# Kernel tuning notes

Hardware: AMD Instinct MI355X
Metric: run time of the kernel (lower is better)

The kernel has to match this reference:

```python
import math
import jax, jax.numpy as jnp
import numpy as np

B, S, CNN_D, LLM_D, BR_D, H = 4, 1024, 512, 768, 1024, 16
PW, CW = 0.2, 0.15  # physics_weight, conservation_weight


def _ln(x, g, b, eps=1e-5):
    m = jnp.mean(x, axis=-1, keepdims=True)
    v = jnp.var(x, axis=-1, keepdims=True)
    return (x - m) * jax.lax.rsqrt(v + eps) * g + b


def _mha(x, wqkv, bqkv, wo, bo, h=H):
    # torch nn.MultiheadAttention (batch_first, self-attention, eval mode)
    Bb, Ss, E = x.shape
    d = E // h
    qkv = x @ wqkv.T + bqkv
    q, k, v = jnp.split(qkv, 3, axis=-1)
    sh = lambda t: t.reshape(Bb, Ss, h, d).transpose(0, 2, 1, 3)
    q, k, v = sh(q), sh(k), sh(v)
    a = jax.nn.softmax(jnp.einsum('bhqd,bhkd->bhqk', q, k) / math.sqrt(d), axis=-1)
    o = jnp.einsum('bhqk,bhkd->bhqd', a, v).transpose(0, 2, 1, 3).reshape(Bb, Ss, E)
    return o @ wo.T + bo


def _phys_attn(qx, kx, wq, bq, wk, bk, wv, bv, wo, bo, g, be, h=H):
    # PhysicsInformedAttention._physics_attention (requires Sq == Sk for the bias broadcast)
    Bb, Sq, E = qx.shape
    Sk = kx.shape[1]
    d = E // h
    Q = (qx @ wq.T + bq).reshape(Bb, Sq, h, d).transpose(0, 2, 1, 3)
    K = (kx @ wk.T + bk).reshape(Bb, Sk, h, d).transpose(0, 2, 1, 3)
    V = (kx @ wv.T + bv).reshape(Bb, Sk, h, d).transpose(0, 2, 1, 3)
    scores = jnp.einsum('bhqd,bhkd->bhqk', Q, K) / math.sqrt(d)
    energy_bias = jnp.sum(Q * K, axis=-1, keepdims=True) * PW   # [B,H,S,1]
    mass_bias = jnp.mean(Q + K, axis=-1, keepdims=True) * CW    # [B,H,S,1]
    a = jax.nn.softmax(scores + energy_bias + mass_bias, axis=-1)
    o = jnp.einsum('bhqk,bhkd->bhqd', a, V).transpose(0, 2, 1, 3).reshape(Bb, Sq, E)
    return _ln(qx + (o @ wo.T + bo), g, be)


def _bridge(x, w, b, g, be):
    # Linear -> GELU (exact) -> LayerNorm (Dropout is no-op in eval)
    return _ln(jax.nn.gelu(x @ w.T + b, approximate=False), g, be)


def setup_inputs() -> dict:
    key = jax.random.key(0)
    ks = iter(jax.random.split(key, 64))
    nrm = lambda *s: jax.random.normal(next(ks), s, jnp.float32)
    w = lambda *s: nrm(*s) * 0.02
    return dict(
        datacube=nrm(B, 5, 8, 16, 16),
        llm_features=nrm(B, S, LLM_D),
        enhanced_cnn_features=nrm(B, S, CNN_D),
        sa_wqkv=w(3 * CNN_D, CNN_D), sa_bqkv=jnp.zeros(3 * CNN_D),
        sa_wo=w(CNN_D, CNN_D), sa_bo=jnp.zeros(CNN_D),
        ta_wqkv=w(3 * CNN_D, CNN_D), ta_bqkv=jnp.zeros(3 * CNN_D),
        ta_wo=w(CNN_D, CNN_D), ta_bo=jnp.zeros(CNN_D),
        c2b_w=w(BR_D, CNN_D), c2b_b=jnp.zeros(BR_D), c2b_g=jnp.ones(BR_D), c2b_be=jnp.zeros(BR_D),
        l2b_w=w(BR_D, LLM_D), l2b_b=jnp.zeros(BR_D), l2b_g=jnp.ones(BR_D), l2b_be=jnp.zeros(BR_D),
        pq_w=w(BR_D, BR_D), pq_b=jnp.zeros(BR_D),
        pk_w=w(BR_D, BR_D), pk_b=jnp.zeros(BR_D),
        pv_w=w(BR_D, BR_D), pv_b=jnp.zeros(BR_D),
        po_w=w(BR_D, BR_D), po_b=jnp.zeros(BR_D),
        e_emb=nrm(1, 1, BR_D), m_emb=nrm(1, 1, BR_D), p_emb=nrm(1, 1, BR_D),
        pa_g=jnp.ones(BR_D), pa_be=jnp.zeros(BR_D),
        c2l_w=w(LLM_D, BR_D), c2l_b=jnp.zeros(LLM_D), c2l_g=jnp.ones(LLM_D), c2l_be=jnp.zeros(LLM_D),
        l2c_w=w(CNN_D, BR_D), l2c_b=jnp.zeros(CNN_D), l2c_g=jnp.ones(CNN_D), l2c_be=jnp.zeros(CNN_D),
    )


def reference(datacube, llm_features, enhanced_cnn_features,
              sa_wqkv, sa_bqkv, sa_wo, sa_bo,
              ta_wqkv, ta_bqkv, ta_wo, ta_bo,
              c2b_w, c2b_b, c2b_g, c2b_be,
              l2b_w, l2b_b, l2b_g, l2b_be,
              pq_w, pq_b, pk_w, pk_b, pv_w, pv_b, po_w, po_b,
              e_emb, m_emb, p_emb, pa_g, pa_be,
              c2l_w, c2l_b, c2l_g, c2l_be,
              l2c_w, l2c_b, l2c_g, l2c_be):
    # enhanced_cnn_features path bypasses the conv3d processor
    cnn = enhanced_cnn_features                       # [B,S,512]
    cnn = cnn + _mha(cnn, sa_wqkv, sa_bqkv, sa_wo, sa_bo)   # spatial integration
    cnn = cnn + _mha(cnn, ta_wqkv, ta_bqkv, ta_wo, ta_bo)   # temporal integration
    cnn_b = _bridge(cnn, c2b_w, c2b_b, c2b_g, c2b_be)       # [B,S,1024]
    llm_b = _bridge(llm_features, l2b_w, l2b_b, l2b_g, l2b_be)  # [B,S,1024]
    phys = jnp.broadcast_to(jnp.concatenate([e_emb, m_emb, p_emb], axis=1),
                            (cnn.shape[0], 3, BR_D))
    aug_cnn = jnp.concatenate([cnn_b, phys], axis=1)  # [B,S+3,1024]
    aug_llm = jnp.concatenate([llm_b, phys], axis=1)
    cnn_att = _phys_attn(aug_cnn, aug_llm, pq_w, pq_b, pk_w, pk_b, pv_w, pv_b,
                         po_w, po_b, pa_g, pa_be)[:, :S]
    llm_att = _phys_attn(aug_llm, aug_cnn, pq_w, pq_b, pk_w, pk_b, pv_w, pv_b,
                         po_w, po_b, pa_g, pa_be)[:, :S]
    llm_enhanced = _bridge(cnn_att, c2l_w, c2l_b, c2l_g, c2l_be)  # cnn->llm bridge [B,S,768]
    cnn_enhanced = _bridge(llm_att, l2c_w, l2c_b, l2c_g, l2c_be)  # llm->cnn bridge [B,S,512]
    return (cnn_enhanced, llm_enhanced)
```

## Files before the change

kernel.cpp:

```cpp
#include <hip/hip_runtime.h>
#include <cstdint>
#include <cstddef>

#define B_    4
#define S_    1024
#define CNN_DIM 512
#define LLM_DIM 768
#define BR_DIM  1024
#define NH    16
#define SAUG  1027

typedef __attribute__((ext_vector_type(8))) short short8;
typedef __attribute__((ext_vector_type(4))) float f32x4;
typedef __attribute__((ext_vector_type(4))) unsigned short us4;
typedef unsigned short u16;
typedef unsigned int u32;
typedef unsigned long long u64;

__device__ __forceinline__ float bf2f(u16 h) {
    union { u32 u; float f; } c; c.u = ((u32)h) << 16; return c.f;
}
__device__ __forceinline__ u16 f2bf(float f) {
    union { u32 u; float f; } c; c.f = f;
    return (u16)((c.u + 0x7FFFu + ((c.u >> 16) & 1u)) >> 16);
}
__device__ __forceinline__ short f2bfS(float f) { return (short)f2bf(f); }
__device__ __forceinline__ u32 cvt_pk_bf16(float lo, float hi) {
    u32 r;
    asm("v_cvt_pk_bf16_f32 %0, %1, %2" : "=v"(r) : "v"(lo), "v"(hi));
    return r;
}

#define GLLDS(gp, lp) __builtin_amdgcn_global_load_lds( \
    (const __attribute__((address_space(1))) void*)(gp), \
    (__attribute__((address_space(3))) void*)(lp), 16, 0, 0)

#define NCONV 14
struct ConvArgs { const float* src[NCONV]; u16* dst[NCONV]; int cum[NCONV + 1]; };

__global__ __launch_bounds__(256) void convert_many(ConvArgs a, int total4) {
    int idx = blockIdx.x * 256 + threadIdx.x;
    if (idx >= total4) return;
    int seg = 0;
#pragma unroll
    for (int i = 1; i < NCONV; i++) if (a.cum[i] <= idx) seg = i;
    int j = idx - a.cum[seg];
    float4 v = ((const float4*)a.src[seg])[j];
    us4 o;
    o[0] = f2bf(v.x); o[1] = f2bf(v.y); o[2] = f2bf(v.z); o[3] = f2bf(v.w);
    ((us4*)a.dst[seg])[j] = o;
}

template<int RESID>
__global__ __launch_bounds__(256) void gemm2_kernel(
    const u16* __restrict__ A, const u16* __restrict__ W,
    const float* __restrict__ bias, const void* __restrict__ residp,
    u16* __restrict__ C, int M, int N, int K)
{
    __shared__ u16 smA[2][64 * 64];
    __shared__ u16 smB[2][128 * 64];

    const int tid = threadIdx.x;
    const int lane = tid & 63;
    const int w = tid >> 6;
    const int wm = w & 1, wn = w >> 1;
    const int mi = lane & 15, g = lane >> 4;
    const int m0 = blockIdx.y * 64;
    const int n0 = blockIdx.x * 128;
    const int lrow = lane >> 3;
    const int lcol = lane & 7;

    f32x4 acc[2][4] = {};
    const int nk = K >> 6;
    int cur = 0;

    auto stage = [&](int buf, int kt) {
        const int kbase = kt * 64;
#pragma unroll
        for (int i = 0; i < 6; i++) {
            int c = w * 6 + i;
            if (c < 8) {
                int row = c * 8 + lrow;
                int col16 = lcol ^ (row & 7);
                int grow = m0 + row; if (grow > M - 1) grow = M - 1;
                GLLDS(A + (size_t)grow * K + kbase + col16 * 8, &smA[buf][c * 512]);
            } else {
                int c8 = c - 8;
                int row = c8 * 8 + lrow;
                int col16 = lcol ^ (row & 7);
                GLLDS(W + (size_t)(n0 + row) * K + kbase + col16 * 8, &smB[buf][c8 * 512]);
            }
        }
    };

    stage(0, 0);
    __syncthreads();

    for (int kt = 0; kt < nk; ++kt) {
        if (kt + 1 < nk) stage(cur ^ 1, kt + 1);
#pragma unroll
        for (int h = 0; h < 2; h++) {
            short8 af[2], bf[4];
#pragma unroll
            for (int im = 0; im < 2; im++) {
                int row = wm * 32 + im * 16 + mi;
                af[im] = *(const short8*)&smA[cur][row * 64 + ((h * 4 + g) ^ (mi & 7)) * 8];
            }
#pragma unroll
            for (int in = 0; in < 4; in++) {
                int row = wn * 64 + in * 16 + mi;
                bf[in] = *(const short8*)&smB[cur][row * 64 + ((h * 4 + g) ^ (mi & 7)) * 8];
            }
#pragma unroll
            for (int im = 0; im < 2; im++)
#pragma unroll
                for (int in = 0; in < 4; in++)
                    acc[im][in] = __builtin_amdgcn_mfma_f32_16x16x32_bf16(af[im], bf[in], acc[im][in], 0, 0, 0);
        }
        __syncthreads();
        cur ^= 1;
    }

#pragma unroll
    for (int im = 0; im < 2; im++) {
#pragma unroll
        for (int r = 0; r < 4; r++) {
            int row = m0 + wm * 32 + im * 16 + g * 4 + r;
            if (row >= M) continue;
            size_t base = (size_t)row * N;
#pragma unroll
            for (int in = 0; in < 4; in++) {
                int col = n0 + wn * 64 + in * 16 + mi;
                float v = acc[im][in][r] + bias[col];
                if (RESID == 1) v += bf2f(((const u16*)residp)[base + col]);
                if (RESID == 2) v += ((const float*)residp)[base + col];
                C[base + col] = f2bf(v);
            }
        }
    }
}

template<int DH, bool SPLIT>
__global__ __launch_bounds__(256) void transpose_v(
    const u16* __restrict__ Vin, u16* __restrict__ VTa, u16* __restrict__ VTb,
    int Sk, int in_rs, long long in_bs, int KPAD)
{
    __shared__ u16 tile[64][DH + 8];
    const int tid = threadIdx.x;
    const int gb = blockIdx.z, h = blockIdx.y;
    const int k0 = blockIdx.x * 64;
    const u16* src = Vin + (size_t)gb * in_bs + h * DH;

    constexpr int CH = DH / 8;
    for (int i = tid; i < 64 * CH; i += 256) {
        int key = i / CH, c = i % CH;
        short8 v = {0,0,0,0,0,0,0,0};
        if (k0 + key < Sk) v = *(const short8*)(src + (size_t)(k0 + key) * in_rs + c * 8);
        *(short8*)&tile[key][c * 8] = v;
    }
    __syncthreads();

    u16* base;
    if (SPLIT) base = (gb < 4) ? (VTa + ((size_t)(gb * NH + h) * DH) * KPAD)
                               : (VTb + ((size_t)((gb - 4) * NH + h) * DH) * KPAD);
    else       base = VTa + ((size_t)(gb * NH + h) * DH) * KPAD;
    u16* dst = base + k0;
    for (int i = tid; i < DH * 8; i += 256) {
        int d = i >> 3, c = i & 7;
        short8 o;
#pragma unroll
        for (int j = 0; j < 8; j++) o[j] = (short)tile[c * 8 + j][d];
        *(short8*)(dst + (size_t)d * KPAD + c * 8) = o;
    }
}

template<int DH, bool PHYS>
__global__ __launch_bounds__(256) void attn7(
    const u16* __restrict__ Q, const u16* __restrict__ Kb,
    const u16* __restrict__ VTa, const u16* __restrict__ VTb,
    u16* __restrict__ Ob, int Sk, int q_rs, int kv_rs, int o_rs,
    long long q_bs, long long kv_bs, long long o_bs, int KPAD, float scale)
{
    constexpr int KT = 32;
    constexpr int NDB = DH / 16;
    constexpr int NCH = DH / 32;
    constexpr int KLDP = DH + 8;
    constexpr int VLDP = 40;
    __shared__ __align__(16) u16 Kt[KT][KLDP];
    __shared__ __align__(16) u16 Vt[DH][VLDP];
    __shared__ __align__(16) u64 Px[4][16][10];

    const int tid = threadIdx.x;
    const int lane = tid & 63;
    const int w = tid >> 6;
    const int mi = lane & 15, g = lane >> 4;
    const int z = blockIdx.z, h = blockIdx.y;
    const int hoff = h * DH;
    const int qw = blockIdx.x * 64 + w * 16;
    const float sc2 = scale * 1.44269504088896f;

    int kb, vg;
    const u16* vts;
    if (PHYS) {
        kb = (z < 4) ? z + 4 : z - 4;
        vts = (z < 4) ? VTb : VTa;
        vg = (z < 4) ? z : z - 4;
    } else { kb = z; vts = VTa; vg = z; }

    int krow, kseg; bool kact;
    int vd, vks;   bool vact;
    if (DH == 64) { krow = tid >> 3; kseg = tid & 7; kact = true;
                    vd = tid >> 2;   vks = tid & 3;  vact = true; }
    else          { krow = tid >> 2; kseg = tid & 3; kact = (tid < 128);
                    vd = (tid - 128) >> 2; vks = tid & 3; vact = (tid >= 128); }

    short8 qfrag[NCH];
    {
        const u16* qs = Q + (size_t)z * q_bs + (size_t)(qw + mi) * q_rs + hoff + g * 8;
#pragma unroll
        for (int c = 0; c < NCH; c++) {
            short8 q8 = *(const short8*)(qs + 32 * c);
#pragma unroll
            for (int j = 0; j < 8; j++) q8[j] = f2bfS(bf2f((u16)q8[j]) * sc2);
            qfrag[c] = q8;
        }
    }

    const short one = (short)0x3F80;
    const short8 ones8 = {one, one, one, one, one, one, one, one};

    f32x4 acc[NDB] = {};
    f32x4 accl = {0.f, 0.f, 0.f, 0.f};
    const u16* kbb = Kb + (size_t)kb * kv_bs + hoff;
    const u16* vtb = vts + ((size_t)(vg * NH + h) * DH) * KPAD;

    const int nt = (Sk + KT - 1) / KT;

    short8 kr8 = {0,0,0,0,0,0,0,0}, vr8 = {0,0,0,0,0,0,0,0};
    auto loadKV = [&](int t) {
        if (kact) {
            int key = t * KT + krow; if (key > Sk - 1) key = Sk - 1;
            kr8 = *(const short8*)(kbb + (size_t)key * kv_rs + kseg * 8);
        }
        if (vact)
            vr8 = *(const short8*)(vtb + (size_t)vd * KPAD + t * KT + vks * 8);
    };

    loadKV(0);

    for (int t = 0; t < nt; t++) {
        const int rem = Sk - t * KT;
        __syncthreads();
        if (kact) *(short8*)&Kt[krow][kseg * 8] = kr8;
        if (vact) *(short8*)&Vt[vd][vks * 8] = vr8;
        __syncthreads();
        if (t + 1 < nt) loadKV(t + 1);

        f32x4 sA = {0,0,0,0}, sB = {0,0,0,0};
#pragma unroll
        for (int c = 0; c < NCH; c++) {
            short8 ka = *(const short8*)&Kt[mi][g * 8 + 32 * c];
            short8 kb8 = *(const short8*)&Kt[16 + mi][g * 8 + 32 * c];
            sA = __builtin_amdgcn_mfma_f32_16x16x32_bf16(ka, qfrag[c], sA, 0, 0, 0);
            sB = __builtin_amdgcn_mfma_f32_16x16x32_bf16(kb8, qfrag[c], sB, 0, 0, 0);
        }

        float pa[4], pb[4];
        if (rem >= KT) {
#pragma unroll
            for (int r = 0; r < 4; r++) {
                pa[r] = exp2f(sA[r]);
                pb[r] = exp2f(sB[r]);
            }
        } else {
#pragma unroll
            for (int r = 0; r < 4; r++) {
                pa[r] = (4 * g + r < rem)      ? exp2f(sA[r]) : 0.f;
                pb[r] = (16 + 4 * g + r < rem) ? exp2f(sB[r]) : 0.f;
            }
        }

        {
            uint2 wa, wb;
            wa.x = cvt_pk_bf16(pa[0], pa[1]);
            wa.y = cvt_pk_bf16(pa[2], pa[3]);
            wb.x = cvt_pk_bf16(pb[0], pb[1]);
            wb.y = cvt_pk_bf16(pb[2], pb[3]);
            uint2* prow = (uint2*)&Px[w][mi][0];
            prow[g] = wa;
            prow[4 + g] = wb;
        }
        short8 pfrag = *(const short8*)((const u16*)&Px[w][mi][0] + 8 * g);

        accl = __builtin_amdgcn_mfma_f32_16x16x32_bf16(ones8, pfrag, accl, 0, 0, 0);

#pragma unroll
        for (int db = 0; db < NDB; db++) {
            short8 vf = *(const short8*)&Vt[db * 16 + mi][g * 8];
            acc[db] = __builtin_amdgcn_mfma_f32_16x16x32_bf16(vf, pfrag, acc[db], 0, 0, 0);
        }
    }

    const float inv = 1.f / accl[0];
    u16* obase = Ob + (size_t)z * o_bs + (size_t)(qw + mi) * o_rs + hoff;
#pragma unroll
    for (int db = 0; db < NDB; db++)
#pragma unroll
        for (int r = 0; r < 4; r++)
            obase[db * 16 + 4 * g + r] = f2bf(acc[db][r] * inv);
}

template<bool GELU, bool RESID, bool OUTF32>
__global__ __launch_bounds__(256) void ln_kernel(
    const u16* __restrict__ X, const u16* __restrict__ resid,
    const float* __restrict__ gg, const float* __restrict__ be,
    void* __restrict__ out, int N, int rows_per_batch,
    long long resid_bs, int resid_rs, long long out_bs, int out_rs)
{
    __shared__ float buf[1024];
    __shared__ float red[2][4];
    __shared__ float stat[2];
    const int row = blockIdx.x;
    const int b = row / rows_per_batch, r = row % rows_per_batch;
    const int tid = threadIdx.x, lane = tid & 63, w = tid >> 6;
    const u16* xr = X + (size_t)row * N;
    const u16* rr = RESID ? (resid + (size_t)b * resid_bs + (size_t)r * resid_rs) : (const u16*)nullptr;

    float s = 0.f, s2 = 0.f;
    for (int i0 = tid * 4; i0 < N; i0 += 1024) {
        us4 xv = *(const us4*)(xr + i0);
        us4 rv = {0,0,0,0};
        if (RESID) rv = *(const us4*)(rr + i0);
        float4 xb;
        float* xp = &xb.x;
#pragma unroll
        for (int u = 0; u < 4; u++) {
            float x = bf2f(xv[u]);
            if (RESID) x += bf2f(rv[u]);
            if (GELU)  x = 0.5f * x * (1.f + erff(x * 0.70710678118654752f));
            xp[u] = x; s += x; s2 += x * x;
        }
        *(float4*)&buf[i0] = xb;
    }
#pragma unroll
    for (int off = 32; off; off >>= 1) { s += __shfl_xor(s, off); s2 += __shfl_xor(s2, off); }
    if (lane == 0) { red[0][w] = s; red[1][w] = s2; }
    __syncthreads();
    if (tid == 0) {
        float a = red[0][0] + red[0][1] + red[0][2] + red[0][3];
        float q = red[1][0] + red[1][1] + red[1][2] + red[1][3];
        float mean = a / N;
        float var = q / N - mean * mean;
        stat[0] = mean; stat[1] = rsqrtf(var + 1e-5f);
    }
    __syncthreads();
    const float mean = stat[0], rs = stat[1];
    const size_t obase = (size_t)b * out_bs + (size_t)r * out_rs;
    for (int i0 = tid * 4; i0 < N; i0 += 1024) {
        if (OUTF32) {
            float4 o;
            o.x = (buf[i0+0] - mean) * rs * gg[i0+0] + be[i0+0];
            o.y = (buf[i0+1] - mean) * rs * gg[i0+1] + be[i0+1];
            o.z = (buf[i0+2] - mean) * rs * gg[i0+2] + be[i0+2];
            o.w = (buf[i0+3] - mean) * rs * gg[i0+3] + be[i0+3];
            *(float4*)((float*)out + obase + i0) = o;
        } else {
            us4 o;
#pragma unroll
            for (int u = 0; u < 4; u++)
                o[u] = f2bf((buf[i0+u] - mean) * rs * gg[i0+u] + be[i0+u]);
            *(us4*)((u16*)out + obase + i0) = o;
        }
    }
}

__global__ __launch_bounds__(256) void fill_phys_kernel(
    const float* __restrict__ e, const float* __restrict__ m, const float* __restrict__ p,
    u16* __restrict__ augc, u16* __restrict__ augl)
{
    int i = blockIdx.x * 256 + threadIdx.x;
    if (i >= 3 * BR_DIM) return;
    int r = i / BR_DIM, j = i % BR_DIM;
    u16 v = f2bf((r == 0) ? e[j] : (r == 1) ? m[j] : p[j]);
#pragma unroll
    for (int b = 0; b < B_; b++) {
        size_t off = ((size_t)b * SAUG + S_ + r) * BR_DIM + j;
        augc[off] = v; augl[off] = v;
    }
}

template<int RESID>
static void gemm(hipStream_t s, const u16* A, const u16* W, const float* bias,
                 const void* resid, u16* C, int M, int N, int K)
{
    dim3 grid(N / 128, (M + 63) / 64), block(256);
    gemm2_kernel<RESID><<<grid, block, 0, s>>>(A, W, bias, resid, C, M, N, K);
}

extern "C" void kernel_launch(void* const* d_in, const int* in_sizes, int n_in,
                              void* d_out, int out_size, void* d_ws, size_t ws_size,
                              hipStream_t stream)
{
    auto F = [&](int i) { return (const float*)d_in[i]; };
    uint8_t* ws = (uint8_t*)d_ws;

    u16* W_SA_QKV = (u16*)(ws + 256);
    u16* W_SA_O   = (u16*)(ws + 1573120);
    u16* W_TA_QKV = (u16*)(ws + 2097408);
    u16* W_TA_O   = (u16*)(ws + 3670272);
    u16* W_C2B    = (u16*)(ws + 4194560);
    u16* W_L2B    = (u16*)(ws + 5243136);
    u16* W_PQ     = (u16*)(ws + 6816000);
    u16* W_PK     = (u16*)(ws + 8913152);
    u16* W_PV     = (u16*)(ws + 11010304);
    u16* W_PO     = (u16*)(ws + 13107456);
    u16* W_C2L    = (u16*)(ws + 15204608);
    u16* W_L2C    = (u16*)(ws + 16777472);
    u16* VT32     = (u16*)(ws + 17826048);
    u16* CNN_B    = (u16*)(ws + 17826048);
    u16* LLM_B    = (u16*)(ws + 22020352);
    u16* QKV      = (u16*)(ws + 28311808);
    u16* ATT      = (u16*)(ws + 40894720);
    u16* CNN1     = (u16*)(ws + 45089024);
    u16* CNN2     = (u16*)(ws + 49283328);
    u16* AUGC     = (u16*)(ws + 53477632);
    u16* AUGL     = (u16*)(ws + 61890816);
    u16* VTA      = (u16*)(ws + 17826048);
    u16* PV_ALL   = (u16*)(ws + 26738944);
    u16* VTB      = (u16*)(ws + 43565312);
    u16* OB_ALL   = (u16*)(ws + 26738944);
    u16* PQ_ALL   = (u16*)(ws + 70304000);
    u16* PK_ALL   = (u16*)(ws + 87130368);
    u16* X8       = QKV;
    u16* X8_ALL   = (u16*)(ws + 70304000);
    u16* CATT_ALL = (u16*)(ws + 87130368);
    u16* X6       = (u16*)(ws + 26738944);
    u16* X4       = (u16*)(ws + 26738944);
    float* outp   = (float*)d_out;

    ConvArgs ca;
    const float* srcs[NCONV] = { F(1), F(2), F(3), F(5), F(7), F(9), F(11),
                                 F(15), F(19), F(21), F(23), F(25), F(32), F(36) };
    u16* dsts[NCONV] = { LLM_B, CNN_B, W_SA_QKV, W_SA_O, W_TA_QKV, W_TA_O, W_C2B,
                         W_L2B, W_PQ, W_PK, W_PV, W_PO, W_C2L, W_L2C };
    const int ns[NCONV] = { 3145728, 2097152, 786432, 262144, 786432, 262144, 524288,
                            786432, 1048576, 1048576, 1048576, 1048576, 786432, 524288 };
    int cum = 0;
    for (int i = 0; i < NCONV; i++) { ca.src[i] = srcs[i]; ca.dst[i] = dsts[i]; ca.cum[i] = cum; cum += ns[i] / 4; }
    ca.cum[NCONV] = cum;
    convert_many<<<(cum + 255) / 256, 256, 0, stream>>>(ca, cum);

    const int M4 = B_ * S_;
    const int MA = B_ * SAUG;
    const float sc32 = 0.17677669529663687f;
    const float sc64 = 0.125f;
    const long long bsQKV = (long long)S_ * 3 * CNN_DIM;
    const long long bsATT = (long long)S_ * CNN_DIM;
    const long long bsAUG = (long long)SAUG * BR_DIM;
    const long long bsO   = (long long)S_ * BR_DIM;
    const int KP32 = 1024;
    const int KP64 = 1088;
    dim3 ablock(256);
    dim3 agrid4(S_ / 64, NH, B_), agrid8(S_ / 64, NH, 2 * B_);
    dim3 tgrid32(16, NH, B_), tgrid64(17, NH, 2 * B_);

    gemm<0>(stream, CNN_B, W_SA_QKV, F(4), nullptr, QKV, M4, 3 * CNN_DIM, CNN_DIM);
    transpose_v<32, false><<<tgrid32, 256, 0, stream>>>(QKV + 2 * CNN_DIM, VT32, nullptr, S_, 3 * CNN_DIM, bsQKV, KP32);
    attn7<32, false><<<agrid4, ablock, 0, stream>>>(QKV, QKV + CNN_DIM, VT32, nullptr, ATT,
        S_, 3 * CNN_DIM, 3 * CNN_DIM, CNN_DIM, bsQKV, bsQKV, bsATT, KP32, sc32);
    gemm<2>(stream, ATT, W_SA_O, F(6), F(2), CNN1, M4, CNN_DIM, CNN_DIM);

    gemm<0>(stream, CNN1, W_TA_QKV, F(8), nullptr, QKV, M4, 3 * CNN_DIM, CNN_DIM);
    transpose_v<32, false><<<tgrid32, 256, 0, stream>>>(QKV + 2 * CNN_DIM, VT32, nullptr, S_, 3 * CNN_DIM, bsQKV, KP32);
    attn7<32, false><<<agrid4, ablock, 0, stream>>>(QKV, QKV + CNN_DIM, VT32, nullptr, ATT,
        S_, 3 * CNN_DIM, 3 * CNN_DIM, CNN_DIM, bsQKV, bsQKV, bsATT, KP32, sc32);
    gemm<1>(stream, ATT, W_TA_O, F(10), CNN1, CNN2, M4, CNN_DIM, CNN_DIM);

    gemm<0>(stream, LLM_B, W_L2B, F(16), nullptr, X8, M4, BR_DIM, LLM_DIM);
    ln_kernel<true, false, false><<<M4, 256, 0, stream>>>(X8, nullptr, F(17), F(18), AUGL,
        BR_DIM, S_, 0, 0, bsAUG, BR_DIM);
    gemm<0>(stream, CNN2, W_C2B, F(12), nullptr, X8, M4, BR_DIM, CNN_DIM);
    ln_kernel<true, false, false><<<M4, 256, 0, stream>>>(X8, nullptr, F(13), F(14), AUGC,
        BR_DIM, S_, 0, 0, bsAUG, BR_DIM);
    fill_phys_kernel<<<12, 256, 0, stream>>>(F(27), F(28), F(29), AUGC, AUGL);

    gemm<0>(stream, AUGC, W_PQ, F(20), nullptr, PQ_ALL, 2 * MA, BR_DIM, BR_DIM);
    gemm<0>(stream, AUGC, W_PK, F(22), nullptr, PK_ALL, 2 * MA, BR_DIM, BR_DIM);
    gemm<0>(stream, AUGC, W_PV, F(24), nullptr, PV_ALL, 2 * MA, BR_DIM, BR_DIM);
    transpose_v<64, true><<<tgrid64, 256, 0, stream>>>(PV_ALL, VTA, VTB, SAUG, BR_DIM, bsAUG, KP64);

    attn7<64, true><<<agrid8, ablock, 0, stream>>>(PQ_ALL, PK_ALL, VTA, VTB, OB_ALL,
        SAUG, BR_DIM, BR_DIM, BR_DIM, bsAUG, bsAUG, bsO, KP64, sc64);

    gemm<0>(stream, OB_ALL, W_PO, F(26), nullptr, X8_ALL, 2 * M4, BR_DIM, BR_DIM);
    ln_kernel<false, true, false><<<2 * M4, 256, 0, stream>>>(X8_ALL, AUGC, F(30), F(31), CATT_ALL,
        BR_DIM, S_, bsAUG, BR_DIM, bsO, BR_DIM);

    gemm<0>(stream, CATT_ALL, W_C2L, F(33), nullptr, X6, M4, LLM_DIM, BR_DIM);
    ln_kernel<true, false, true><<<M4, 256, 0, stream>>>(X6, nullptr, F(34), F(35),
        (void*)(outp + 2097152), LLM_DIM, S_, 0, 0, (long long)S_ * LLM_DIM, LLM_DIM);
    gemm<0>(stream, CATT_ALL + (size_t)M4 * BR_DIM, W_L2C, F(37), nullptr, X4, M4, CNN_DIM, BR_DIM);
    ln_kernel<true, false, true><<<M4, 256, 0, stream>>>(X4, nullptr, F(38), F(39),
        (void*)outp, CNN_DIM, S_, 0, 0, (long long)S_ * CNN_DIM, CNN_DIM);
}
```

Measured before the change: 471.4 us.

## Add 128x128 GEMM tile for large M and process two query groups per attention block

Adds a gemm3 kernel with 128x128 tiles, double-buffered LDS loads and XOR-swizzled shared memory, used when M >= 8192 (the physics projection GEMMs with 2*B*(S+3) rows). The attention kernel now handles two 64-query groups per block, reusing each K/V tile loaded into LDS across both groups and halving the attention grid. Both changes aim to cut global/LDS traffic per FLOP. In exchange they raise register pressure and lower block counts, which may reduce occupancy.

```diff
diff --git a/kernel.cpp b/kernel.cpp
--- a/kernel.cpp
+++ b/kernel.cpp
@@ -140,6 +140,95 @@
     }
 }
 
+template<int RESID>
+__global__ __launch_bounds__(256) void gemm3_kernel(
+    const u16* __restrict__ A, const u16* __restrict__ W,
+    const float* __restrict__ bias, const void* __restrict__ residp,
+    u16* __restrict__ C, int M, int N, int K)
+{
+    __shared__ u16 smA[2][128 * 64];
+    __shared__ u16 smB[2][128 * 64];
+
+    const int tid = threadIdx.x;
+    const int lane = tid & 63;
+    const int w = tid >> 6;
+    const int wm = w & 1, wn = w >> 1;
+    const int mi = lane & 15, g = lane >> 4;
+    const int m0 = blockIdx.y * 128;
+    const int n0 = blockIdx.x * 128;
+    const int lrow = lane >> 3;
+    const int lcol = lane & 7;
+
+    f32x4 acc[4][4] = {};
+    const int nk = K >> 6;
+    int cur = 0;
+
+    auto stage = [&](int buf, int kt) {
+        const int kbase = kt * 64;
+#pragma unroll
+        for (int i = 0; i < 4; i++) {
+            int c = w * 4 + i;
+            int row = c * 8 + lrow;
+            int col16 = lcol ^ (row & 7);
+            int grow = m0 + row; if (grow > M - 1) grow = M - 1;
+            GLLDS(A + (size_t)grow * K + kbase + col16 * 8, &smA[buf][c * 512]);
+        }
+#pragma unroll
+        for (int i = 0; i < 4; i++) {
+            int c = w * 4 + i;
+            int row = c * 8 + lrow;
+            int col16 = lcol ^ (row & 7);
+            GLLDS(W + (size_t)(n0 + row) * K + kbase + col16 * 8, &smB[buf][c * 512]);
+        }
+    };
+
+    stage(0, 0);
+    __syncthreads();
+
+    for (int kt = 0; kt < nk; ++kt) {
+        if (kt + 1 < nk) stage(cur ^ 1, kt + 1);
+#pragma unroll
+        for (int h = 0; h < 2; h++) {
+            short8 af[4], bf[4];
+#pragma unroll
+            for (int im = 0; im < 4; im++) {
+                int row = wm * 64 + im * 16 + mi;
+                af[im] = *(const short8*)&smA[cur][row * 64 + ((h * 4 + g) ^ (mi & 7)) * 8];
+            }
+#pragma unroll
+            for (int in = 0; in < 4; in++) {
+                int row = wn * 64 + in * 16 + mi;
+                bf[in] = *(const short8*)&smB[cur][row * 64 + ((h * 4 + g) ^ (mi & 7)) * 8];
+            }
+#pragma unroll
+            for (int im = 0; im < 4; im++)
+#pragma unroll
+                for (int in = 0; in < 4; in++)
+                    acc[im][in] = __builtin_amdgcn_mfma_f32_16x16x32_bf16(af[im], bf[in], acc[im][in], 0, 0, 0);
+        }
+        __syncthreads();
+        cur ^= 1;
+    }
+
+#pragma unroll
+    for (int im = 0; im < 4; im++) {
+#pragma unroll
+        for (int r = 0; r < 4; r++) {
+            int row = m0 + wm * 64 + im * 16 + g * 4 + r;
+            if (row >= M) continue;
+            size_t base = (size_t)row * N;
+#pragma unroll
+            for (int in = 0; in < 4; in++) {
+                int col = n0 + wn * 64 + in * 16 + mi;
+                float v = acc[im][in][r] + bias[col];
+                if (RESID == 1) v += bf2f(((const u16*)residp)[base + col]);
+                if (RESID == 2) v += ((const float*)residp)[base + col];
+                C[base + col] = f2bf(v);
+            }
+        }
+    }
+}
+
 template<int DH, bool SPLIT>
 __global__ __launch_bounds__(256) void transpose_v(
     const u16* __restrict__ Vin, u16* __restrict__ VTa, u16* __restrict__ VTb,
@@ -174,8 +263,8 @@
     }
 }
 
-template<int DH, bool PHYS>
-__global__ __launch_bounds__(256) void attn7(
+template<int DH, bool PHYS, int QG>
+__global__ __launch_bounds__(256) void attn8(
     const u16* __restrict__ Q, const u16* __restrict__ Kb,
     const u16* __restrict__ VTa, const u16* __restrict__ VTb,
     u16* __restrict__ Ob, int Sk, int q_rs, int kv_rs, int o_rs,
@@ -196,7 +285,7 @@
     const int mi = lane & 15, g = lane >> 4;
     const int z = blockIdx.z, h = blockIdx.y;
     const int hoff = h * DH;
-    const int qw = blockIdx.x * 64 + w * 16;
+    const int qw = blockIdx.x * (64 * QG) + w * 16;
     const float sc2 = scale * 1.44269504088896f;
 
     int kb, vg;
@@ -214,23 +303,24 @@
     else          { krow = tid >> 2; kseg = tid & 3; kact = (tid < 128);
                     vd = (tid - 128) >> 2; vks = tid & 3; vact = (tid >= 128); }
 
-    short8 qfrag[NCH];
-    {
-        const u16* qs = Q + (size_t)z * q_bs + (size_t)(qw + mi) * q_rs + hoff + g * 8;
+    short8 qfrag[QG][NCH];
+#pragma unroll
+    for (int qg = 0; qg < QG; qg++) {
+        const u16* qs = Q + (size_t)z * q_bs + (size_t)(qw + qg * 64 + mi) * q_rs + hoff + g * 8;
 #pragma unroll
         for (int c = 0; c < NCH; c++) {
             short8 q8 = *(const short8*)(qs + 32 * c);
 #pragma unroll
             for (int j = 0; j < 8; j++) q8[j] = f2bfS(bf2f((u16)q8[j]) * sc2);
-            qfrag[c] = q8;
+            qfrag[qg][c] = q8;
         }
     }
 
     const short one = (short)0x3F80;
     const short8 ones8 = {one, one, one, one, one, one, one, one};
 
-    f32x4 acc[NDB] = {};
-    f32x4 accl = {0.f, 0.f, 0.f, 0.f};
+    f32x4 acc[QG][NDB] = {};
+    f32x4 accl[QG] = {};
     const u16* kbb = Kb + (size_t)kb * kv_bs + hoff;
     const u16* vtb = vts + ((size_t)(vg * NH + h) * DH) * KPAD;
 
@@ -256,58 +346,69 @@
         __syncthreads();
         if (t + 1 < nt) loadKV(t + 1);
 
-        f32x4 sA = {0,0,0,0}, sB = {0,0,0,0};
+        short8 ka[NCH], kb8[NCH], vf[NDB];
 #pragma unroll
         for (int c = 0; c < NCH; c++) {
-            short8 ka = *(const short8*)&Kt[mi][g * 8 + 32 * c];
-            short8 kb8 = *(const short8*)&Kt[16 + mi][g * 8 + 32 * c];
-            sA = __builtin_amdgcn_mfma_f32_16x16x32_bf16(ka, qfrag[c], sA, 0, 0, 0);
-            sB = __builtin_amdgcn_mfma_f32_16x16x32_bf16(kb8, qfrag[c], sB, 0, 0, 0);
-        }
-
-        float pa[4], pb[4];
-        if (rem >= KT) {
-#pragma unroll
-            for (int r = 0; r < 4; r++) {
-                pa[r] = exp2f(sA[r]);
-                pb[r] = exp2f(sB[r]);
-            }
-        } else {
-#pragma unroll
-            for (int r = 0; r < 4; r++) {
-                pa[r] = (4 * g + r < rem)      ? exp2f(sA[r]) : 0.f;
-                pb[r] = (16 + 4 * g + r < rem) ? exp2f(sB[r]) : 0.f;
-            }
-        }
-
-        {
-            uint2 wa, wb;
-            wa.x = cvt_pk_bf16(pa[0], pa[1]);
-            wa.y = cvt_pk_bf16(pa[2], pa[3]);
-            wb.x = cvt_pk_bf16(pb[0], pb[1]);
-            wb.y = cvt_pk_bf16(pb[2], pb[3]);
-            uint2* prow = (uint2*)&Px[w][mi][0];
-            prow[g] = wa;
-            prow[4 + g] = wb;
-        }
-        short8 pfrag = *(const short8*)((const u16*)&Px[w][mi][0] + 8 * g);
-
-        accl = __builtin_amdgcn_mfma_f32_16x16x32_bf16(ones8, pfrag, accl, 0, 0, 0);
-
-#pragma unroll
-        for (int db = 0; db < NDB; db++) {
-            short8 vf = *(const short8*)&Vt[db * 16 + mi][g * 8];
-            acc[db] = __builtin_amdgcn_mfma_f32_16x16x32_bf16(vf, pfrag, acc[db], 0, 0, 0);
-        }
-    }
-
-    const float inv = 1.f / accl[0];
-    u16* obase = Ob + (size_t)z * o_bs + (size_t)(qw + mi) * o_rs + hoff;
-#pragma unroll
-    for (int db = 0; db < NDB; db++)
-#pragma unroll
-        for (int r = 0; r < 4; r++)
-            obase[db * 16 + 4 * g + r] = f2bf(acc[db][r] * inv);
+            ka[c]  = *(const short8*)&Kt[mi][g * 8 + 32 * c];
+            kb8[c] = *(const short8*)&Kt[16 + mi][g * 8 + 32 * c];
+        }
+#pragma unroll
+        for (int db = 0; db < NDB; db++)
+            vf[db] = *(const short8*)&Vt[db * 16 + mi][g * 8];
+
+#pragma unroll
+        for (int qg = 0; qg < QG; qg++) {
+            f32x4 sA = {0,0,0,0}, sB = {0,0,0,0};
+#pragma unroll
+            for (int c = 0; c < NCH; c++) {
+                sA = __builtin_amdgcn_mfma_f32_16x16x32_bf16(ka[c],  qfrag[qg][c], sA, 0, 0, 0);
+                sB = __builtin_amdgcn_mfma_f32_16x16x32_bf16(kb8[c], qfrag[qg][c], sB, 0, 0, 0);
+            }
+
+            float pa[4], pb[4];
+            if (rem >= KT) {
+#pragma unroll
+                for (int r = 0; r < 4; r++) {
+                    pa[r] = exp2f(sA[r]);
+                    pb[r] = exp2f(sB[r]);
+                }
+            } else {
+#pragma unroll
+                for (int r = 0; r < 4; r++) {
+                    pa[r] = (4 * g + r < rem)      ? exp2f(sA[r]) : 0.f;
+                    pb[r] = (16 + 4 * g + r < rem) ? exp2f(sB[r]) : 0.f;
+                }
+            }
+
+            {
+                uint2 wa, wb;
+                wa.x = cvt_pk_bf16(pa[0], pa[1]);
+                wa.y = cvt_pk_bf16(pa[2], pa[3]);
+                wb.x = cvt_pk_bf16(pb[0], pb[1]);
+                wb.y = cvt_pk_bf16(pb[2], pb[3]);
+                uint2* prow = (uint2*)&Px[w][mi][0];
+                prow[g] = wa;
+                prow[4 + g] = wb;
+            }
+            short8 pfrag = *(const short8*)((const u16*)&Px[w][mi][0] + 8 * g);
+
+            accl[qg] = __builtin_amdgcn_mfma_f32_16x16x32_bf16(ones8, pfrag, accl[qg], 0, 0, 0);
+#pragma unroll
+            for (int db = 0; db < NDB; db++)
+                acc[qg][db] = __builtin_amdgcn_mfma_f32_16x16x32_bf16(vf[db], pfrag, acc[qg][db], 0, 0, 0);
+        }
+    }
+
+#pragma unroll
+    for (int qg = 0; qg < QG; qg++) {
+        const float inv = 1.f / accl[qg][0];
+        u16* obase = Ob + (size_t)z * o_bs + (size_t)(qw + qg * 64 + mi) * o_rs + hoff;
+#pragma unroll
+        for (int db = 0; db < NDB; db++)
+#pragma unroll
+            for (int r = 0; r < 4; r++)
+                obase[db * 16 + 4 * g + r] = f2bf(acc[qg][db][r] * inv);
+    }
 }
 
 template<bool GELU, bool RESID, bool OUTF32>
@@ -393,8 +494,13 @@
 static void gemm(hipStream_t s, const u16* A, const u16* W, const float* bias,
                  const void* resid, u16* C, int M, int N, int K)
 {
-    dim3 grid(N / 128, (M + 63) / 64), block(256);
-    gemm2_kernel<RESID><<<grid, block, 0, s>>>(A, W, bias, resid, C, M, N, K);
+    if (M >= 8192) {
+        dim3 grid(N / 128, (M + 127) / 128), block(256);
+        gemm3_kernel<RESID><<<grid, block, 0, s>>>(A, W, bias, resid, C, M, N, K);
+    } else {
+        dim3 grid(N / 128, (M + 63) / 64), block(256);
+        gemm2_kernel<RESID><<<grid, block, 0, s>>>(A, W, bias, resid, C, M, N, K);
+    }
 }
 
 extern "C" void kernel_launch(void* const* d_in, const int* in_sizes, int n_in,
@@ -461,18 +567,18 @@
     const int KP32 = 1024;
     const int KP64 = 1088;
     dim3 ablock(256);
-    dim3 agrid4(S_ / 64, NH, B_), agrid8(S_ / 64, NH, 2 * B_);
+    dim3 agrid4(S_ / 128, NH, B_), agrid8(S_ / 128, NH, 2 * B_);
     dim3 tgrid32(16, NH, B_), tgrid64(17, NH, 2 * B_);
 
     gemm<0>(stream, CNN_B, W_SA_QKV, F(4), nullptr, QKV, M4, 3 * CNN_DIM, CNN_DIM);
     transpose_v<32, false><<<tgrid32, 256, 0, stream>>>(QKV + 2 * CNN_DIM, VT32, nullptr, S_, 3 * CNN_DIM, bsQKV, KP32);
-    attn7<32, false><<<agrid4, ablock, 0, stream>>>(QKV, QKV + CNN_DIM, VT32, nullptr, ATT,
+    attn8<32, false, 2><<<agrid4, ablock, 0, stream>>>(QKV, QKV + CNN_DIM, VT32, nullptr, ATT,
         S_, 3 * CNN_DIM, 3 * CNN_DIM, CNN_DIM, bsQKV, bsQKV, bsATT, KP32, sc32);
     gemm<2>(stream, ATT, W_SA_O, F(6), F(2), CNN1, M4, CNN_DIM, CNN_DIM);
 
     gemm<0>(stream, CNN1, W_TA_QKV, F(8), nullptr, QKV, M4, 3 * CNN_DIM, CNN_DIM);
     transpose_v<32, false><<<tgrid32, 256, 0, stream>>>(QKV + 2 * CNN_DIM, VT32, nullptr, S_, 3 * CNN_DIM, bsQKV, KP32);
-    attn7<32, false><<<agrid4, ablock, 0, stream>>>(QKV, QKV + CNN_DIM, VT32, nullptr, ATT,
+    attn8<32, false, 2><<<agrid4, ablock, 0, stream>>>(QKV, QKV + CNN_DIM, VT32, nullptr, ATT,
         S_, 3 * CNN_DIM, 3 * CNN_DIM, CNN_DIM, bsQKV, bsQKV, bsATT, KP32, sc32);
     gemm<1>(stream, ATT, W_TA_O, F(10), CNN1, CNN2, M4, CNN_DIM, CNN_DIM);
 
@@ -489,7 +595,7 @@
     gemm<0>(stream, AUGC, W_PV, F(24), nullptr, PV_ALL, 2 * MA, BR_DIM, BR_DIM);
     transpose_v<64, true><<<tgrid64, 256, 0, stream>>>(PV_ALL, VTA, VTB, SAUG, BR_DIM, bsAUG, KP64);
 
-    attn7<64, true><<<agrid8, ablock, 0, stream>>>(PQ_ALL, PK_ALL, VTA, VTB, OB_ALL,
+    attn8<64, true, 2><<<agrid8, ablock, 0, stream>>>(PQ_ALL, PK_ALL, VTA, VTB, OB_ALL,
         SAUG, BR_DIM, BR_DIM, BR_DIM, bsAUG, bsAUG, bsO, KP64, sc64);
 
     gemm<0>(stream, OB_ALL, W_PO, F(26), nullptr, X8_ALL, 2 * M4, BR_DIM, BR_DIM);
```

Result: slower. 481.6 us (+2.2%).

## Process multiple query groups per attention block and fuse Q/K projection GEMMs

Applied to the files above, without the earlier changes.

The attention kernel now handles QG query tiles of 64 rows per block (2 for the small heads, 4 for the physics heads), so each K/V tile loaded into shared memory serves more queries. The K and V fragments are hoisted into registers once per tile and reused across the query groups. Separately, the Q and K projections are merged into one GEMM with N=2048, which relies on W_PQ and W_PK being stored next to each other and on a combined bias buffer filled by a new small kernel. The cost is more registers per thread and fewer blocks in the attention grid, which may lower occupancy.

```diff
diff --git a/kernel.cpp b/kernel.cpp
--- a/kernel.cpp
+++ b/kernel.cpp
@@ -49,6 +49,14 @@
     us4 o;
     o[0] = f2bf(v.x); o[1] = f2bf(v.y); o[2] = f2bf(v.z); o[3] = f2bf(v.w);
     ((us4*)a.dst[seg])[j] = o;
+}
+
+__global__ __launch_bounds__(256) void fill_bias2(
+    const float* __restrict__ b0, const float* __restrict__ b1, float* __restrict__ out)
+{
+    int i = blockIdx.x * 256 + threadIdx.x;
+    if (i < 1024) out[i] = b0[i];
+    else if (i < 2048) out[i] = b1[i - 1024];
 }
 
 template<int RESID>
@@ -174,8 +182,8 @@
     }
 }
 
-template<int DH, bool PHYS>
-__global__ __launch_bounds__(256) void attn7(
+template<int DH, bool PHYS, int QG>
+__global__ __launch_bounds__(256) void attn8(
     const u16* __restrict__ Q, const u16* __restrict__ Kb,
     const u16* __restrict__ VTa, const u16* __restrict__ VTb,
     u16* __restrict__ Ob, int Sk, int q_rs, int kv_rs, int o_rs,
@@ -196,7 +204,7 @@
     const int mi = lane & 15, g = lane >> 4;
     const int z = blockIdx.z, h = blockIdx.y;
     const int hoff = h * DH;
-    const int qw = blockIdx.x * 64 + w * 16;
+    const int qw = blockIdx.x * (64 * QG) + w * 16;
     const float sc2 = scale * 1.44269504088896f;
 
     int kb, vg;
@@ -214,23 +222,24 @@
     else          { krow = tid >> 2; kseg = tid & 3; kact = (tid < 128);
                     vd = (tid - 128) >> 2; vks = tid & 3; vact = (tid >= 128); }
 
-    short8 qfrag[NCH];
-    {
-        const u16* qs = Q + (size_t)z * q_bs + (size_t)(qw + mi) * q_rs + hoff + g * 8;
+    short8 qfrag[QG][NCH];
+#pragma unroll
+    for (int qg = 0; qg < QG; qg++) {
+        const u16* qs = Q + (size_t)z * q_bs + (size_t)(qw + qg * 64 + mi) * q_rs + hoff + g * 8;
 #pragma unroll
         for (int c = 0; c < NCH; c++) {
             short8 q8 = *(const short8*)(qs + 32 * c);
 #pragma unroll
             for (int j = 0; j < 8; j++) q8[j] = f2bfS(bf2f((u16)q8[j]) * sc2);
-            qfrag[c] = q8;
+            qfrag[qg][c] = q8;
         }
     }
 
     const short one = (short)0x3F80;
     const short8 ones8 = {one, one, one, one, one, one, one, one};
 
-    f32x4 acc[NDB] = {};
-    f32x4 accl = {0.f, 0.f, 0.f, 0.f};
+    f32x4 acc[QG][NDB] = {};
+    f32x4 accl[QG] = {};
     const u16* kbb = Kb + (size_t)kb * kv_bs + hoff;
     const u16* vtb = vts + ((size_t)(vg * NH + h) * DH) * KPAD;
 
@@ -256,58 +265,69 @@
         __syncthreads();
         if (t + 1 < nt) loadKV(t + 1);
 
-        f32x4 sA = {0,0,0,0}, sB = {0,0,0,0};
+        short8 ka[NCH], kb8[NCH], vf[NDB];
 #pragma unroll
         for (int c = 0; c < NCH; c++) {
-            short8 ka = *(const short8*)&Kt[mi][g * 8 + 32 * c];
-            short8 kb8 = *(const short8*)&Kt[16 + mi][g * 8 + 32 * c];
-            sA = __builtin_amdgcn_mfma_f32_16x16x32_bf16(ka, qfrag[c], sA, 0, 0, 0);
-            sB = __builtin_amdgcn_mfma_f32_16x16x32_bf16(kb8, qfrag[c], sB, 0, 0, 0);
-        }
-
-        float pa[4], pb[4];
-        if (rem >= KT) {
-#pragma unroll
-            for (int r = 0; r < 4; r++) {
-                pa[r] = exp2f(sA[r]);
-                pb[r] = exp2f(sB[r]);
-            }
-        } else {
-#pragma unroll
-            for (int r = 0; r < 4; r++) {
-                pa[r] = (4 * g + r < rem)      ? exp2f(sA[r]) : 0.f;
-                pb[r] = (16 + 4 * g + r < rem) ? exp2f(sB[r]) : 0.f;
-            }
-        }
-
-        {
-            uint2 wa, wb;
-            wa.x = cvt_pk_bf16(pa[0], pa[1]);
-            wa.y = cvt_pk_bf16(pa[2], pa[3]);
-            wb.x = cvt_pk_bf16(pb[0], pb[1]);
-            wb.y = cvt_pk_bf16(pb[2], pb[3]);
-            uint2* prow = (uint2*)&Px[w][mi][0];
-            prow[g] = wa;
-            prow[4 + g] = wb;
-        }
-        short8 pfrag = *(const short8*)((const u16*)&Px[w][mi][0] + 8 * g);
-
-        accl = __builtin_amdgcn_mfma_f32_16x16x32_bf16(ones8, pfrag, accl, 0, 0, 0);
-
-#pragma unroll
-        for (int db = 0; db < NDB; db++) {
-            short8 vf = *(const short8*)&Vt[db * 16 + mi][g * 8];
-            acc[db] = __builtin_amdgcn_mfma_f32_16x16x32_bf16(vf, pfrag, acc[db], 0, 0, 0);
-        }
-    }
-
-    const float inv = 1.f / accl[0];
-    u16* obase = Ob + (size_t)z * o_bs + (size_t)(qw + mi) * o_rs + hoff;
-#pragma unroll
-    for (int db = 0; db < NDB; db++)
-#pragma unroll
-        for (int r = 0; r < 4; r++)
-            obase[db * 16 + 4 * g + r] = f2bf(acc[db][r] * inv);
+            ka[c]  = *(const short8*)&Kt[mi][g * 8 + 32 * c];
+            kb8[c] = *(const short8*)&Kt[16 + mi][g * 8 + 32 * c];
+        }
+#pragma unroll
+        for (int db = 0; db < NDB; db++)
+            vf[db] = *(const short8*)&Vt[db * 16 + mi][g * 8];
+
+#pragma unroll
+        for (int qg = 0; qg < QG; qg++) {
+            f32x4 sA = {0,0,0,0}, sB = {0,0,0,0};
+#pragma unroll
+            for (int c = 0; c < NCH; c++) {
+                sA = __builtin_amdgcn_mfma_f32_16x16x32_bf16(ka[c],  qfrag[qg][c], sA, 0, 0, 0);
+                sB = __builtin_amdgcn_mfma_f32_16x16x32_bf16(kb8[c], qfrag[qg][c], sB, 0, 0, 0);
+            }
+
+            float pa[4], pb[4];
+            if (rem >= KT) {
+#pragma unroll
+                for (int r = 0; r < 4; r++) {
+                    pa[r] = exp2f(sA[r]);
+                    pb[r] = exp2f(sB[r]);
+                }
+            } else {
+#pragma unroll
+                for (int r = 0; r < 4; r++) {
+                    pa[r] = (4 * g + r < rem)      ? exp2f(sA[r]) : 0.f;
+                    pb[r] = (16 + 4 * g + r < rem) ? exp2f(sB[r]) : 0.f;
+                }
+            }
+
+            {
+                uint2 wa, wb;
+                wa.x = cvt_pk_bf16(pa[0], pa[1]);
+                wa.y = cvt_pk_bf16(pa[2], pa[3]);
+                wb.x = cvt_pk_bf16(pb[0], pb[1]);
+                wb.y = cvt_pk_bf16(pb[2], pb[3]);
+                uint2* prow = (uint2*)&Px[w][mi][0];
+                prow[g] = wa;
+                prow[4 + g] = wb;
+            }
+            short8 pfrag = *(const short8*)((const u16*)&Px[w][mi][0] + 8 * g);
+
+            accl[qg] = __builtin_amdgcn_mfma_f32_16x16x32_bf16(ones8, pfrag, accl[qg], 0, 0, 0);
+#pragma unroll
+            for (int db = 0; db < NDB; db++)
+                acc[qg][db] = __builtin_amdgcn_mfma_f32_16x16x32_bf16(vf[db], pfrag, acc[qg][db], 0, 0, 0);
+        }
+    }
+
+#pragma unroll
+    for (int qg = 0; qg < QG; qg++) {
+        const float inv = 1.f / accl[qg][0];
+        u16* obase = Ob + (size_t)z * o_bs + (size_t)(qw + qg * 64 + mi) * o_rs + hoff;
+#pragma unroll
+        for (int db = 0; db < NDB; db++)
+#pragma unroll
+            for (int r = 0; r < 4; r++)
+                obase[db * 16 + 4 * g + r] = f2bf(acc[qg][db][r] * inv);
+    }
 }
 
 template<bool GELU, bool RESID, bool OUTF32>
@@ -428,9 +448,9 @@
     u16* VTA      = (u16*)(ws + 17826048);
     u16* PV_ALL   = (u16*)(ws + 26738944);
     u16* VTB      = (u16*)(ws + 43565312);
+    float* BIAS2  = (float*)(ws + 52478208);
     u16* OB_ALL   = (u16*)(ws + 26738944);
-    u16* PQ_ALL   = (u16*)(ws + 70304000);
-    u16* PK_ALL   = (u16*)(ws + 87130368);
+    u16* PQK_ALL  = (u16*)(ws + 70304000);
     u16* X8       = QKV;
     u16* X8_ALL   = (u16*)(ws + 70304000);
     u16* CATT_ALL = (u16*)(ws + 87130368);
@@ -449,6 +469,7 @@
     for (int i = 0; i < NCONV; i++) { ca.src[i] = srcs[i]; ca.dst[i] = dsts[i]; ca.cum[i] = cum; cum += ns[i] / 4; }
     ca.cum[NCONV] = cum;
     convert_many<<<(cum + 255) / 256, 256, 0, stream>>>(ca, cum);
+    fill_bias2<<<8, 256, 0, stream>>>(F(20), F(22), BIAS2);
 
     const int M4 = B_ * S_;
     const int MA = B_ * SAUG;
@@ -457,22 +478,23 @@
     const long long bsQKV = (long long)S_ * 3 * CNN_DIM;
     const long long bsATT = (long long)S_ * CNN_DIM;
     const long long bsAUG = (long long)SAUG * BR_DIM;
+    const long long bsPQK = (long long)SAUG * 2048;
     const long long bsO   = (long long)S_ * BR_DIM;
     const int KP32 = 1024;
     const int KP64 = 1088;
     dim3 ablock(256);
-    dim3 agrid4(S_ / 64, NH, B_), agrid8(S_ / 64, NH, 2 * B_);
+    dim3 agrid4(S_ / 128, NH, B_), agrid8(S_ / 256, NH, 2 * B_);
     dim3 tgrid32(16, NH, B_), tgrid64(17, NH, 2 * B_);
 
     gemm<0>(stream, CNN_B, W_SA_QKV, F(4), nullptr, QKV, M4, 3 * CNN_DIM, CNN_DIM);
     transpose_v<32, false><<<tgrid32, 256, 0, stream>>>(QKV + 2 * CNN_DIM, VT32, nullptr, S_, 3 * CNN_DIM, bsQKV, KP32);
-    attn7<32, false><<<agrid4, ablock, 0, stream>>>(QKV, QKV + CNN_DIM, VT32, nullptr, ATT,
+    attn8<32, false, 2><<<agrid4, ablock, 0, stream>>>(QKV, QKV + CNN_DIM, VT32, nullptr, ATT,
         S_, 3 * CNN_DIM, 3 * CNN_DIM, CNN_DIM, bsQKV, bsQKV, bsATT, KP32, sc32);
     gemm<2>(stream, ATT, W_SA_O, F(6), F(2), CNN1, M4, CNN_DIM, CNN_DIM);
 
     gemm<0>(stream, CNN1, W_TA_QKV, F(8), nullptr, QKV, M4, 3 * CNN_DIM, CNN_DIM);
     transpose_v<32, false><<<tgrid32, 256, 0, stream>>>(QKV + 2 * CNN_DIM, VT32, nullptr, S_, 3 * CNN_DIM, bsQKV, KP32);
-    attn7<32, false><<<agrid4, ablock, 0, stream>>>(QKV, QKV + CNN_DIM, VT32, nullptr, ATT,
+    attn8<32, false, 2><<<agrid4, ablock, 0, stream>>>(QKV, QKV + CNN_DIM, VT32, nullptr, ATT,
         S_, 3 * CNN_DIM, 3 * CNN_DIM, CNN_DIM, bsQKV, bsQKV, bsATT, KP32, sc32);
     gemm<1>(stream, ATT, W_TA_O, F(10), CNN1, CNN2, M4, CNN_DIM, CNN_DIM);
 
@@ -484,13 +506,12 @@
         BR_DIM, S_, 0, 0, bsAUG, BR_DIM);
     fill_phys_kernel<<<12, 256, 0, stream>>>(F(27), F(28), F(29), AUGC, AUGL);
 
-    gemm<0>(stream, AUGC, W_PQ, F(20), nullptr, PQ_ALL, 2 * MA, BR_DIM, BR_DIM);
-    gemm<0>(stream, AUGC, W_PK, F(22), nullptr, PK_ALL, 2 * MA, BR_DIM, BR_DIM);
+    gemm<0>(stream, AUGC, W_PQ, BIAS2, nullptr, PQK_ALL, 2 * MA, 2048, BR_DIM);
     gemm<0>(stream, AUGC, W_PV, F(24), nullptr, PV_ALL, 2 * MA, BR_DIM, BR_DIM);
     transpose_v<64, true><<<tgrid64, 256, 0, stream>>>(PV_ALL, VTA, VTB, SAUG, BR_DIM, bsAUG, KP64);
 
-    attn7<64, true><<<agrid8, ablock, 0, stream>>>(PQ_ALL, PK_ALL, VTA, VTB, OB_ALL,
-        SAUG, BR_DIM, BR_DIM, BR_DIM, bsAUG, bsAUG, bsO, KP64, sc64);
+    attn8<64, true, 4><<<agrid8, ablock, 0, stream>>>(PQK_ALL, PQK_ALL + 1024, VTA, VTB, OB_ALL,
+        SAUG, 2048, 2048, BR_DIM, bsPQK, bsPQK, bsO, KP64, sc64);
 
     gemm<0>(stream, OB_ALL, W_PO, F(26), nullptr, X8_ALL, 2 * M4, BR_DIM, BR_DIM);
     ln_kernel<false, true, false><<<2 * M4, 256, 0, stream>>>(X8_ALL, AUGC, F(30), F(31), CATT_ALL,
```

Result: faster. 459.6 us (-2.5%).
